# Kernel optimization log

Measured on AMD Instinct MI355X. Metric: run time of the kernel, lower is better.

Reference implementation:

```python
import jax, jax.numpy as jnp
import numpy as np
from jax.scipy.special import erf, erfinv

N_OBS = 8192   # number of observations
N_LOC = 2048   # number of spatial locations (q)


def setup_inputs() -> dict:
    key = jax.random.key(0)
    k1, k2, k3, k4 = jax.random.split(key, 4)
    # random 2-D coordinates -> symmetric pairwise squared-distance matrix (zero diag)
    coords = jax.random.uniform(k1, (N_LOC, 2), dtype=jnp.float32) * 10.0
    dist_matrix = jnp.sum((coords[:, None, :] - coords[None, :, :]) ** 2, axis=-1)  # [q,q]
    Z_idx = jax.random.randint(k2, (N_OBS,), 0, N_LOC)                              # location id per obs
    y_true = jax.random.normal(k3, (N_OBS, 1), dtype=jnp.float32)
    y_pred = jax.random.normal(k4, (N_OBS, 1), dtype=jnp.float32) * 0.5
    return {
        "y_true": y_true,
        "y_pred": y_pred,
        "Z_idx": Z_idx,
        "dist_matrix": dist_matrix,
        "sig2e": jnp.array([1.0], dtype=jnp.float32),
        "sig2bs": jnp.array([0.5], dtype=jnp.float32),
        "lengthscale": jnp.array([2.0], dtype=jnp.float32),
    }


def _inverse_gaussian_cdf(u):
    # tf.math.erfinv(2*clip(u,1e-5,1-1e-5)-1) * sqrt(2)
    return erfinv(2.0 * jnp.clip(u, 1e-5, 1.0 - 1e-5) - 1.0) * jnp.sqrt(2.0)


def reference(y_true, y_pred, Z_idx, dist_matrix, sig2e, sig2bs, lengthscale):
    N = y_true.shape[0]
    q = dist_matrix.shape[0]
    dt = y_true.dtype
    # getD: exponential distance kernel over locations  D = sig2b * exp(-M / (2*ell))
    D = sig2bs[0] * jnp.exp(-dist_matrix / (2.0 * lengthscale[0]))          # [q,q]
    # getZ: dense one-hot design matrix (sparse.to_dense of SparseTensor of ones)
    Z = jax.nn.one_hot(Z_idx, q, dtype=dt)                                   # [N,q]
    # V_batch: V = Z D Z' + sig2e * I
    V = Z @ (D @ Z.T) + sig2e[0] * jnp.eye(N, dtype=dt)                      # [N,N]
    sd = jnp.sqrt(jnp.diagonal(V))                                           # sd_sqrt_V
    R = V / (sd[:, None] * sd[None, :])                                      # correlation matrix
    # Gaussian marginal: sig2 = sig2e + sig2b (diag of V)
    sig2 = sig2e[0] + sig2bs[0]
    resid = y_true - y_pred                                                  # [N,1]
    # distribution.cdf_batch: standard normal CDF of resid / sqrt(sig2)
    u = 0.5 * (erf(resid / jnp.sqrt(2.0 * sig2)) + 1.0)
    m = _inverse_gaussian_cdf(u)                                             # [N,1]
    # distribution.sum_log_pdf_batch: sum of Gaussian log-pdf
    sum_log_pdf = jnp.sum(-0.5 * jnp.log(2.0 * jnp.pi * sig2) - resid ** 2 / (2.0 * sig2))
    # solve + logdet via a single Cholesky of the correlation matrix
    L = jnp.linalg.cholesky(R)
    V_inv_m = jax.scipy.linalg.cho_solve((L, True), m)                       # R^{-1} m
    logdet = 2.0 * jnp.sum(jnp.log(jnp.diagonal(L)))                         # logdet(V) - 2*sum(log sd)
    mV_invm = m.T @ V_inv_m                                                  # [1,1]
    mtm = m.T @ m                                                            # [1,1]
    total_loss = 0.5 * logdet + 0.5 * mV_invm - 0.5 * mtm + 0.5 * sum_log_pdf
    return total_loss  # [1,1]
```

## Files before the change

### kernel.cpp

```cpp
#include <hip/hip_runtime.h>
#include <math.h>

#define Q 2048
#define NOBS 8192

__device__ __forceinline__ float rl(float v, int l) {
  return __int_as_float(__builtin_amdgcn_readlane(__float_as_int(v), l));
}

__device__ __forceinline__ float block_sum256(float v, volatile float* red) {
  int tid = threadIdx.x;
#pragma unroll
  for (int o = 32; o > 0; o >>= 1) v += __shfl_down(v, o);
  __syncthreads();
  if ((tid & 63) == 0) red[tid >> 6] = v;
  __syncthreads();
  return red[0] + red[1] + red[2] + red[3];
}

__device__ __forceinline__ float chol64_reg(float rr[64], int lane) {
  float dv = 1.0f;
#pragma unroll
  for (int j = 0; j < 64; ++j) {
    float vjj = rl(rr[j], j);
    float invd = rsqrtf(vjj);
    float lij = rr[j] * invd;
    rr[j] = lij;
    if (lane == j) dv = lij;
#pragma unroll
    for (int k = j + 1; k < 64; ++k) rr[k] -= lij * rl(lij, k);
  }
  return dv;
}

__global__ __launch_bounds__(256) void obs_kernel(
    const float* __restrict__ yt, const float* __restrict__ yp,
    const int* __restrict__ zidx, const float* __restrict__ s2e_p,
    const float* __restrict__ s2b_p, float* __restrict__ t,
    int* __restrict__ cnt, float* __restrict__ scal) {
  __shared__ float red[4];
  int i = blockIdx.x * 256 + threadIdx.x;
  float s2e = s2e_p[0], s2b = s2b_p[0];
  float sig2 = s2e + s2b;
  float r = yt[i] - yp[i];
  float e = erff(r * rsqrtf(2.0f * sig2));
  float u = 0.5f * (e + 1.0f);
  u = fminf(fmaxf(u, 1e-5f), 1.0f - 1e-5f);
  float m = erfinvf(2.0f * u - 1.0f) * 1.4142135623730951f;
  float slp = -0.5f * logf(2.0f * 3.14159265358979f * sig2) - r * r / (2.0f * sig2);
  int z = zidx[i];
  atomicAdd(&t[z], m);
  atomicAdd(&cnt[z], 1);
  float s1 = block_sum256(slp, red);
  float s2 = block_sum256(m * m, red);
  if (threadIdx.x == 0) {
    atomicAdd(&scal[0], s1);
    atomicAdd(&scal[1], s2);
  }
}

__global__ __launch_bounds__(256) void build_mv(
    const float* __restrict__ dist, const float* __restrict__ s2e_p,
    const float* __restrict__ s2b_p, const float* __restrict__ ell_p,
    const int* __restrict__ cnt, const float* __restrict__ t,
    float* __restrict__ G, float* __restrict__ z, float* __restrict__ scal) {
  __shared__ float red[4];
  int j = blockIdx.x;
  float s2e = s2e_p[0], s2b = s2b_p[0], ell = ell_p[0];
  float sig2 = s2e + s2b;
  float ratio = s2b / sig2;
  float diag = s2e / sig2;
  float inv2ell = 1.0f / (2.0f * ell);
  float cj = (float)cnt[j];
  const float* drow = dist + (size_t)j * Q;
  float* grow = G + (size_t)j * Q;
  float s = 0.0f;
  for (int k = threadIdx.x; k < Q; k += 256) {
    float e = expf(-drow[k] * inv2ell);
    s += e * t[k];
    float g = sqrtf(cj * (float)cnt[k]) * (ratio * e);
    if (j == k) g += diag;
    grow[k] = g;
  }
  float tot = block_sum256(s, red);
  if (threadIdx.x == 0) {
    float wj = ratio * tot;
    z[j] = sqrtf(cj) * wj;
    atomicAdd(&scal[2], t[j] * wj);
  }
}

__global__ __launch_bounds__(256, 1) void estep(
    float* __restrict__ G, float* __restrict__ z, float* __restrict__ scal,
    int j1, int m, int ntile) {
  __shared__ __align__(16) float shA[64 * 68];
  __shared__ __align__(16) float shB[64 * 68];
  __shared__ __align__(16) float LT[64 * 64];
  __shared__ float invDs[64];
  __shared__ float z1s[64];
  __shared__ float z2s[64];
  int tid = threadIdx.x, bx = blockIdx.x;
  int lane = tid & 63;
  int j0 = j1 - 64;
  int tx = tid & 15, ty = tid >> 4;

  if (bx <= m) {
    bool isdiag = (bx == 0);
    int R0 = j1 + bx * 64;

    if (j1 > 0) {
#pragma unroll
      for (int it = 0; it < 4; ++it) {
        int idx = it * 256 + tid;
        int r = idx >> 4, c4 = (idx & 15) * 4;
        float4 v = *(const float4*)(G + (size_t)(j1 + r) * Q + j0 + c4);
        shA[(c4 + 0) * 68 + r] = v.x; shA[(c4 + 1) * 68 + r] = v.y;
        shA[(c4 + 2) * 68 + r] = v.z; shA[(c4 + 3) * 68 + r] = v.w;
        if (!isdiag) {
          float4 u = *(const float4*)(G + (size_t)(R0 + r) * Q + j0 + c4);
          shB[(c4 + 0) * 68 + r] = u.x; shB[(c4 + 1) * 68 + r] = u.y;
          shB[(c4 + 2) * 68 + r] = u.z; shB[(c4 + 3) * 68 + r] = u.w;
        }
      }
      if (isdiag && tid < 64) z1s[tid] = z[j0 + tid];
      __syncthreads();

      float acc1[4][4] = {{0.f}};
      float acc2[4][4] = {{0.f}};
#pragma unroll 8
      for (int p = 0; p < 64; ++p) {
        float4 a4 = *(const float4*)&shA[p * 68 + ty * 4];
        float4 b4 = *(const float4*)&shA[p * 68 + tx * 4];
        float av[4] = {a4.x, a4.y, a4.z, a4.w};
        float bv[4] = {b4.x, b4.y, b4.z, b4.w};
#pragma unroll
        for (int i = 0; i < 4; ++i)
#pragma unroll
          for (int jj = 0; jj < 4; ++jj) acc2[i][jj] += av[i] * bv[jj];
        if (!isdiag) {
          float4 c4v = *(const float4*)&shB[p * 68 + ty * 4];
          float cv[4] = {c4v.x, c4v.y, c4v.z, c4v.w};
#pragma unroll
          for (int i = 0; i < 4; ++i)
#pragma unroll
            for (int jj = 0; jj < 4; ++jj) acc1[i][jj] += cv[i] * bv[jj];
        }
      }
      if (isdiag) {
        int rw = tid >> 2, part = tid & 3;
        float ssum = 0.f;
        for (int p = part; p < 64; p += 4) ssum += shA[p * 68 + rw] * z1s[p];
        ssum += __shfl_down(ssum, 2);
        ssum += __shfl_down(ssum, 1);
        if (part == 0) z2s[rw] = z[j1 + rw] - ssum;
      }
      __syncthreads();

#pragma unroll
      for (int i = 0; i < 4; ++i) {
        float4 g = *(const float4*)(G + (size_t)(j1 + ty * 4 + i) * Q + j1 + tx * 4);
        shA[(ty * 4 + i) * 68 + tx * 4 + 0] = g.x - acc2[i][0];
        shA[(ty * 4 + i) * 68 + tx * 4 + 1] = g.y - acc2[i][1];
        shA[(ty * 4 + i) * 68 + tx * 4 + 2] = g.z - acc2[i][2];
        shA[(ty * 4 + i) * 68 + tx * 4 + 3] = g.w - acc2[i][3];
        if (!isdiag) {
          float4 h = *(const float4*)(G + (size_t)(R0 + ty * 4 + i) * Q + j1 + tx * 4);
          shB[(ty * 4 + i) * 68 + tx * 4 + 0] = h.x - acc1[i][0];
          shB[(ty * 4 + i) * 68 + tx * 4 + 1] = h.y - acc1[i][1];
          shB[(ty * 4 + i) * 68 + tx * 4 + 2] = h.z - acc1[i][2];
          shB[(ty * 4 + i) * 68 + tx * 4 + 3] = h.w - acc1[i][3];
        }
      }
      __syncthreads();
    } else {
#pragma unroll
      for (int it = 0; it < 4; ++it) {
        int idx = it * 256 + tid;
        int r = idx >> 4, c4 = (idx & 15) * 4;
        float4 g = *(const float4*)(G + (size_t)r * Q + c4);
        shA[r * 68 + c4 + 0] = g.x; shA[r * 68 + c4 + 1] = g.y;
        shA[r * 68 + c4 + 2] = g.z; shA[r * 68 + c4 + 3] = g.w;
        if (!isdiag) {
          float4 h = *(const float4*)(G + (size_t)(R0 + r) * Q + c4);
          shB[r * 68 + c4 + 0] = h.x; shB[r * 68 + c4 + 1] = h.y;
          shB[r * 68 + c4 + 2] = h.z; shB[r * 68 + c4 + 3] = h.w;
        }
      }
      if (isdiag && tid < 64) z2s[tid] = z[tid];
      __syncthreads();
    }

    if (tid < 64) {
      float rr[64];
#pragma unroll
      for (int k4 = 0; k4 < 16; ++k4) {
        float4 v = *(const float4*)&shA[lane * 68 + k4 * 4];
        rr[k4 * 4 + 0] = v.x; rr[k4 * 4 + 1] = v.y;
        rr[k4 * 4 + 2] = v.z; rr[k4 * 4 + 3] = v.w;
      }
      __builtin_amdgcn_s_setprio(1);
      float dv = chol64_reg(rr, lane);
      __builtin_amdgcn_s_setprio(0);
      float myinv = 1.0f / dv;
      if (isdiag) {
        float lg = logf(dv);
#pragma unroll
        for (int o = 32; o > 0; o >>= 1) lg += __shfl_down(lg, o);
        if (lane == 0) atomicAdd(&scal[3], lg);
        float a = z2s[lane];
#pragma unroll
        for (int p = 0; p < 64; ++p) {
          float xp = rl(a, p) * rl(myinv, p);
          if (lane > p) a -= xp * rr[p];
        }
        z[j1 + lane] = a * myinv;
      } else {
        invDs[lane] = myinv;
#pragma unroll
        for (int p = 0; p < 64; ++p)
          LT[p * 64 + lane] = (p < lane) ? rr[p] : 0.0f;
        float rr2[64];
#pragma unroll
        for (int k4 = 0; k4 < 16; ++k4) {
          float4 v = *(const float4*)&shB[lane * 68 + k4 * 4];
          rr2[k4 * 4 + 0] = v.x; rr2[k4 * 4 + 1] = v.y;
          rr2[k4 * 4 + 2] = v.z; rr2[k4 * 4 + 3] = v.w;
        }
        __builtin_amdgcn_s_setprio(1);
#pragma unroll
        for (int p = 0; p < 64; ++p) {
          float xp = rr2[p] * invDs[p];
          rr2[p] = xp;
#pragma unroll
          for (int k4 = 0; k4 < 16; ++k4) {
            if (k4 * 4 + 3 > p) {
              float4 l4 = *(const float4*)&LT[p * 64 + k4 * 4];
              rr2[k4 * 4 + 0] -= xp * l4.x;
              rr2[k4 * 4 + 1] -= xp * l4.y;
              rr2[k4 * 4 + 2] -= xp * l4.z;
              rr2[k4 * 4 + 3] -= xp * l4.w;
            }
          }
        }
        __builtin_amdgcn_s_setprio(0);
#pragma unroll
        for (int k4 = 0; k4 < 16; ++k4) {
          float4 st;
          st.x = rr2[k4 * 4 + 0]; st.y = rr2[k4 * 4 + 1];
          st.z = rr2[k4 * 4 + 2]; st.w = rr2[k4 * 4 + 3];
          *(float4*)(G + (size_t)(R0 + lane) * Q + j1 + k4 * 4) = st;
        }
      }
    }
    return;
  }

  int tjob = bx - (m + 1);
  if (tjob < ntile) {
    int bi = (int)((sqrtf(8.0f * (float)tjob + 1.0f) - 1.0f) * 0.5f);
    while ((bi + 1) * (bi + 2) / 2 <= tjob) ++bi;
    while (bi * (bi + 1) / 2 > tjob) --bi;
    int bk = tjob - bi * (bi + 1) / 2;
    int R0 = j1 + 64 + bi * 64, C0 = j1 + 64 + bk * 64;
    bool sym = (bi == bk);
#pragma unroll
    for (int it = 0; it < 4; ++it) {
      int idx = it * 256 + tid;
      int r = idx >> 4, c4 = (idx & 15) * 4;
      float4 v = *(const float4*)(G + (size_t)(R0 + r) * Q + j0 + c4);
      shA[(c4 + 0) * 68 + r] = v.x; shA[(c4 + 1) * 68 + r] = v.y;
      shA[(c4 + 2) * 68 + r] = v.z; shA[(c4 + 3) * 68 + r] = v.w;
      if (!sym) {
        float4 u = *(const float4*)(G + (size_t)(C0 + r) * Q + j0 + c4);
        shB[(c4 + 0) * 68 + r] = u.x; shB[(c4 + 1) * 68 + r] = u.y;
        shB[(c4 + 2) * 68 + r] = u.z; shB[(c4 + 3) * 68 + r] = u.w;
      }
    }
    __syncthreads();
    const float* sB = sym ? shA : shB;
    float acc[4][4] = {{0.f}};
#pragma unroll 8
    for (int p = 0; p < 64; ++p) {
      float4 a4 = *(const float4*)&shA[p * 68 + ty * 4];
      float4 b4 = *(const float4*)&sB[p * 68 + tx * 4];
      float av[4] = {a4.x, a4.y, a4.z, a4.w};
      float bv[4] = {b4.x, b4.y, b4.z, b4.w};
#pragma unroll
      for (int i = 0; i < 4; ++i)
#pragma unroll
        for (int jj = 0; jj < 4; ++jj) acc[i][jj] += av[i] * bv[jj];
    }
#pragma unroll
    for (int i = 0; i < 4; ++i) {
      float* gp = G + (size_t)(R0 + ty * 4 + i) * Q + C0 + tx * 4;
      float4 g = *(const float4*)gp;
      g.x -= acc[i][0]; g.y -= acc[i][1];
      g.z -= acc[i][2]; g.w -= acc[i][3];
      *(float4*)gp = g;
    }
    return;
  }

  {
    int zb = tjob - ntile;
    int B0 = j1 + 64 + zb * 64;
    if (tid < 64) z1s[tid] = z[j0 + tid];
    __syncthreads();
    int rw = tid >> 2, part = tid & 3;
    const float* Lr = G + (size_t)(B0 + rw) * Q + j0;
    float ssum = 0.f;
    for (int p = part; p < 64; p += 4) ssum += Lr[p] * z1s[p];
    ssum += __shfl_down(ssum, 2);
    ssum += __shfl_down(ssum, 1);
    if (part == 0) z[B0 + rw] -= ssum;
  }
}

__global__ __launch_bounds__(256) void final_assemble(
    const float* __restrict__ z, const float* __restrict__ scal,
    const float* __restrict__ s2e_p, const float* __restrict__ s2b_p,
    float* __restrict__ out) {
  __shared__ float red[4];
  int tid = threadIdx.x;
  float bv = 0.f;
  for (int i = tid; i < Q; i += 256) {
    float zi = z[i];
    bv += zi * zi;
  }
  float bvs = block_sum256(bv, red);
  if (tid == 0) {
    float s2e = s2e_p[0], s2b = s2b_p[0];
    float sig2 = s2e + s2b;
    float c = s2e / sig2;
    float slp = scal[0], mtm = scal[1];
    float tw = scal[2], sl = scal[3];
    float tty = (tw - bvs) / c;
    float mrm = (mtm - tty) / c;
    float logdetR = (float)(NOBS - Q) * logf(c) + 2.0f * sl;
    out[0] = 0.5f * logdetR + 0.5f * mrm - 0.5f * mtm + 0.5f * slp;
  }
}

extern "C" void kernel_launch(void* const* d_in, const int* in_sizes, int n_in,
                              void* d_out, int out_size, void* d_ws, size_t ws_size,
                              hipStream_t stream) {
  const float* yt   = (const float*)d_in[0];
  const float* yp   = (const float*)d_in[1];
  const int*   zidx = (const int*)d_in[2];
  const float* dist = (const float*)d_in[3];
  const float* s2e  = (const float*)d_in[4];
  const float* s2b  = (const float*)d_in[5];
  const float* ell  = (const float*)d_in[6];

  float* ws   = (float*)d_ws;
  float* G    = ws;
  float* z    = ws + (size_t)Q * Q;
  float* t    = z + Q;
  int*   cntv = (int*)(t + Q);
  float* scal = t + 2 * Q;

  hipMemsetAsync(t, 0, (2 * Q + 8) * sizeof(float), stream);

  obs_kernel<<<NOBS / 256, 256, 0, stream>>>(yt, yp, zidx, s2e, s2b, t, cntv, scal);
  build_mv<<<Q, 256, 0, stream>>>(dist, s2e, s2b, ell, cntv, t, G, z, scal);

  estep<<<32, 256, 0, stream>>>(G, z, scal, 0, 31, 0);

  for (int s = 0; s <= 30; ++s) {
    int j1 = (s + 1) * 64;
    int m = 30 - s;
    int ntile = m * (m + 1) / 2;
    estep<<<1 + 2 * m + ntile, 256, 0, stream>>>(G, z, scal, j1, m, ntile);
  }

  final_assemble<<<1, 256, 0, stream>>>(z, scal, s2e, s2b, (float*)d_out);
}
```

Baseline: 1.099 ms.

## Restructure blocked Cholesky into right-looking steps with redundant panel solves

```diff
diff --git a/kernel.cpp b/kernel.cpp
--- a/kernel.cpp
+++ b/kernel.cpp
@@ -31,6 +31,47 @@
     for (int k = j + 1; k < 64; ++k) rr[k] -= lij * rl(lij, k);
   }
   return dv;
+}
+
+__device__ __forceinline__ void panel_solve(float* sh, const float* LT,
+                                            const float* invDs, int lane) {
+  float rr2[64];
+#pragma unroll
+  for (int k = 0; k < 64; ++k) rr2[k] = sh[k * 68 + lane];
+  __builtin_amdgcn_s_setprio(1);
+#pragma unroll
+  for (int p = 0; p < 64; ++p) {
+    float xp = rr2[p] * invDs[p];
+    rr2[p] = xp;
+#pragma unroll
+    for (int k4 = 0; k4 < 16; ++k4) {
+      if (k4 * 4 + 3 > p) {
+        float4 l4 = *(const float4*)&LT[p * 64 + k4 * 4];
+        rr2[k4 * 4 + 0] -= xp * l4.x;
+        rr2[k4 * 4 + 1] -= xp * l4.y;
+        rr2[k4 * 4 + 2] -= xp * l4.z;
+        rr2[k4 * 4 + 3] -= xp * l4.w;
+      }
+    }
+  }
+  __builtin_amdgcn_s_setprio(0);
+#pragma unroll
+  for (int k = 0; k < 64; ++k) sh[k * 68 + lane] = rr2[k];
+}
+
+__device__ __forceinline__ void zsolve(const float* LT, const float* invDs,
+                                       const float* zin, float* z1s, int lane) {
+  float rr3[64];
+#pragma unroll
+  for (int p = 0; p < 64; ++p) rr3[p] = LT[p * 64 + lane];
+  float a = zin[lane];
+  float myinv = invDs[lane];
+#pragma unroll
+  for (int p = 0; p < 64; ++p) {
+    float xp = rl(a, p) * rl(myinv, p);
+    if (lane > p) a -= xp * rr3[p];
+  }
+  z1s[lane] = a * myinv;
 }
 
 __global__ __launch_bounds__(256) void obs_kernel(
@@ -90,241 +131,203 @@
   }
 }
 
+__global__ __launch_bounds__(64, 1) void potrf_first(
+    const float* __restrict__ G, float* __restrict__ dsA,
+    float* __restrict__ scal) {
+  int lane = threadIdx.x;
+  float rr[64];
+  const float* row = G + (size_t)lane * Q;
+#pragma unroll
+  for (int k4 = 0; k4 < 16; ++k4) {
+    float4 v = *(const float4*)(row + k4 * 4);
+    rr[k4 * 4 + 0] = v.x; rr[k4 * 4 + 1] = v.y;
+    rr[k4 * 4 + 2] = v.z; rr[k4 * 4 + 3] = v.w;
+  }
+  float dv = chol64_reg(rr, lane);
+#pragma unroll
+  for (int k4 = 0; k4 < 16; ++k4) {
+    float4 st;
+    st.x = rr[k4 * 4 + 0]; st.y = rr[k4 * 4 + 1];
+    st.z = rr[k4 * 4 + 2]; st.w = rr[k4 * 4 + 3];
+    *(float4*)(dsA + lane * 64 + k4 * 4) = st;
+  }
+  float lg = logf(dv);
+#pragma unroll
+  for (int o = 32; o > 0; o >>= 1) lg += __shfl_down(lg, o);
+  if (lane == 0) atomicAdd(&scal[3], lg);
+}
+
 __global__ __launch_bounds__(256, 1) void estep(
-    float* __restrict__ G, float* __restrict__ z, float* __restrict__ scal,
-    int j1, int m, int ntile) {
+    float* __restrict__ G, float* __restrict__ z, float* __restrict__ z1,
+    float* __restrict__ scal, const float* __restrict__ dsR,
+    float* __restrict__ dsW, int j0) {
   __shared__ __align__(16) float shA[64 * 68];
   __shared__ __align__(16) float shB[64 * 68];
   __shared__ __align__(16) float LT[64 * 64];
   __shared__ float invDs[64];
   __shared__ float z1s[64];
-  __shared__ float z2s[64];
   int tid = threadIdx.x, bx = blockIdx.x;
-  int lane = tid & 63;
-  int j0 = j1 - 64;
+  int lane = tid & 63, wv = tid >> 6;
   int tx = tid & 15, ty = tid >> 4;
-
-  if (bx <= m) {
-    bool isdiag = (bx == 0);
-    int R0 = j1 + bx * 64;
-
-    if (j1 > 0) {
-#pragma unroll
-      for (int it = 0; it < 4; ++it) {
-        int idx = it * 256 + tid;
-        int r = idx >> 4, c4 = (idx & 15) * 4;
-        float4 v = *(const float4*)(G + (size_t)(j1 + r) * Q + j0 + c4);
-        shA[(c4 + 0) * 68 + r] = v.x; shA[(c4 + 1) * 68 + r] = v.y;
-        shA[(c4 + 2) * 68 + r] = v.z; shA[(c4 + 3) * 68 + r] = v.w;
-        if (!isdiag) {
-          float4 u = *(const float4*)(G + (size_t)(R0 + r) * Q + j0 + c4);
-          shB[(c4 + 0) * 68 + r] = u.x; shB[(c4 + 1) * 68 + r] = u.y;
-          shB[(c4 + 2) * 68 + r] = u.z; shB[(c4 + 3) * 68 + r] = u.w;
-        }
-      }
-      if (isdiag && tid < 64) z1s[tid] = z[j0 + tid];
-      __syncthreads();
-
-      float acc1[4][4] = {{0.f}};
-      float acc2[4][4] = {{0.f}};
+  int j1 = j0 + 64;
+
+  bool isjob0 = (bx == 0);
+  int tjob = bx - 1;
+  if (!isjob0 && tjob == 0) return;
+
+  int R0, C0;
+  bool sym;
+  if (isjob0) {
+    R0 = j1; C0 = j1; sym = true;
+  } else {
+    int bi = (int)((sqrtf(8.0f * (float)tjob + 1.0f) - 1.0f) * 0.5f);
+    while ((bi + 1) * (bi + 2) / 2 <= tjob) ++bi;
+    while (bi * (bi + 1) / 2 > tjob) --bi;
+    int bk = tjob - bi * (bi + 1) / 2;
+    R0 = j1 + bi * 64; C0 = j1 + bk * 64; sym = (bi == bk);
+  }
+
+#pragma unroll
+  for (int it = 0; it < 4; ++it) {
+    int idx = it * 256 + tid;
+    int r = idx >> 4, c4 = (idx & 15) * 4;
+    float4 v = *(const float4*)(dsR + r * 64 + c4);
+    LT[(c4 + 0) * 64 + r] = (c4 + 0 < r) ? v.x : 0.0f;
+    LT[(c4 + 1) * 64 + r] = (c4 + 1 < r) ? v.y : 0.0f;
+    LT[(c4 + 2) * 64 + r] = (c4 + 2 < r) ? v.z : 0.0f;
+    LT[(c4 + 3) * 64 + r] = (c4 + 3 < r) ? v.w : 0.0f;
+    if (r >= c4 && r < c4 + 4) {
+      float d = (r == c4) ? v.x : (r == c4 + 1) ? v.y : (r == c4 + 2) ? v.z : v.w;
+      invDs[r] = 1.0f / d;
+    }
+  }
+#pragma unroll
+  for (int it = 0; it < 4; ++it) {
+    int idx = it * 256 + tid;
+    int r = idx >> 4, c4 = (idx & 15) * 4;
+    float4 v = *(const float4*)(G + (size_t)(R0 + r) * Q + j0 + c4);
+    shA[(c4 + 0) * 68 + r] = v.x; shA[(c4 + 1) * 68 + r] = v.y;
+    shA[(c4 + 2) * 68 + r] = v.z; shA[(c4 + 3) * 68 + r] = v.w;
+    if (!sym) {
+      float4 u = *(const float4*)(G + (size_t)(C0 + r) * Q + j0 + c4);
+      shB[(c4 + 0) * 68 + r] = u.x; shB[(c4 + 1) * 68 + r] = u.y;
+      shB[(c4 + 2) * 68 + r] = u.z; shB[(c4 + 3) * 68 + r] = u.w;
+    }
+  }
+  __syncthreads();
+
+  if (wv == 0) {
+    panel_solve(shA, LT, invDs, lane);
+  } else if (wv == 1) {
+    if (!sym) panel_solve(shB, LT, invDs, lane);
+    else      zsolve(LT, invDs, z + j0, z1s, lane);
+  }
+  __syncthreads();
+
+  if (isjob0 && wv == 1) z1[j0 + lane] = z1s[lane];
+
+  const float* sB = sym ? shA : shB;
+  float acc[4][4] = {{0.f}};
 #pragma unroll 8
-      for (int p = 0; p < 64; ++p) {
-        float4 a4 = *(const float4*)&shA[p * 68 + ty * 4];
-        float4 b4 = *(const float4*)&shA[p * 68 + tx * 4];
-        float av[4] = {a4.x, a4.y, a4.z, a4.w};
-        float bv[4] = {b4.x, b4.y, b4.z, b4.w};
-#pragma unroll
-        for (int i = 0; i < 4; ++i)
-#pragma unroll
-          for (int jj = 0; jj < 4; ++jj) acc2[i][jj] += av[i] * bv[jj];
-        if (!isdiag) {
-          float4 c4v = *(const float4*)&shB[p * 68 + ty * 4];
-          float cv[4] = {c4v.x, c4v.y, c4v.z, c4v.w};
-#pragma unroll
-          for (int i = 0; i < 4; ++i)
-#pragma unroll
-            for (int jj = 0; jj < 4; ++jj) acc1[i][jj] += cv[i] * bv[jj];
-        }
-      }
-      if (isdiag) {
-        int rw = tid >> 2, part = tid & 3;
-        float ssum = 0.f;
-        for (int p = part; p < 64; p += 4) ssum += shA[p * 68 + rw] * z1s[p];
-        ssum += __shfl_down(ssum, 2);
-        ssum += __shfl_down(ssum, 1);
-        if (part == 0) z2s[rw] = z[j1 + rw] - ssum;
-      }
-      __syncthreads();
-
-#pragma unroll
-      for (int i = 0; i < 4; ++i) {
-        float4 g = *(const float4*)(G + (size_t)(j1 + ty * 4 + i) * Q + j1 + tx * 4);
-        shA[(ty * 4 + i) * 68 + tx * 4 + 0] = g.x - acc2[i][0];
-        shA[(ty * 4 + i) * 68 + tx * 4 + 1] = g.y - acc2[i][1];
-        shA[(ty * 4 + i) * 68 + tx * 4 + 2] = g.z - acc2[i][2];
-        shA[(ty * 4 + i) * 68 + tx * 4 + 3] = g.w - acc2[i][3];
-        if (!isdiag) {
-          float4 h = *(const float4*)(G + (size_t)(R0 + ty * 4 + i) * Q + j1 + tx * 4);
-          shB[(ty * 4 + i) * 68 + tx * 4 + 0] = h.x - acc1[i][0];
-          shB[(ty * 4 + i) * 68 + tx * 4 + 1] = h.y - acc1[i][1];
-          shB[(ty * 4 + i) * 68 + tx * 4 + 2] = h.z - acc1[i][2];
-          shB[(ty * 4 + i) * 68 + tx * 4 + 3] = h.w - acc1[i][3];
-        }
-      }
-      __syncthreads();
-    } else {
-#pragma unroll
-      for (int it = 0; it < 4; ++it) {
-        int idx = it * 256 + tid;
-        int r = idx >> 4, c4 = (idx & 15) * 4;
-        float4 g = *(const float4*)(G + (size_t)r * Q + c4);
-        shA[r * 68 + c4 + 0] = g.x; shA[r * 68 + c4 + 1] = g.y;
-        shA[r * 68 + c4 + 2] = g.z; shA[r * 68 + c4 + 3] = g.w;
-        if (!isdiag) {
-          float4 h = *(const float4*)(G + (size_t)(R0 + r) * Q + c4);
-          shB[r * 68 + c4 + 0] = h.x; shB[r * 68 + c4 + 1] = h.y;
-          shB[r * 68 + c4 + 2] = h.z; shB[r * 68 + c4 + 3] = h.w;
-        }
-      }
-      if (isdiag && tid < 64) z2s[tid] = z[tid];
-      __syncthreads();
-    }
-
-    if (tid < 64) {
+  for (int p = 0; p < 64; ++p) {
+    float4 a4 = *(const float4*)&shA[p * 68 + ty * 4];
+    float4 b4 = *(const float4*)&sB[p * 68 + tx * 4];
+    float av[4] = {a4.x, a4.y, a4.z, a4.w};
+    float bv[4] = {b4.x, b4.y, b4.z, b4.w};
+#pragma unroll
+    for (int i = 0; i < 4; ++i)
+#pragma unroll
+      for (int jj = 0; jj < 4; ++jj) acc[i][jj] += av[i] * bv[jj];
+  }
+
+  if (isjob0) {
+#pragma unroll
+    for (int i = 0; i < 4; ++i) {
+      const float* gp = G + (size_t)(j1 + ty * 4 + i) * Q + j1 + tx * 4;
+      float4 g = *(const float4*)gp;
+      shB[(ty * 4 + i) * 68 + tx * 4 + 0] = g.x - acc[i][0];
+      shB[(ty * 4 + i) * 68 + tx * 4 + 1] = g.y - acc[i][1];
+      shB[(ty * 4 + i) * 68 + tx * 4 + 2] = g.z - acc[i][2];
+      shB[(ty * 4 + i) * 68 + tx * 4 + 3] = g.w - acc[i][3];
+    }
+    __syncthreads();
+    if (wv == 0) {
       float rr[64];
 #pragma unroll
       for (int k4 = 0; k4 < 16; ++k4) {
-        float4 v = *(const float4*)&shA[lane * 68 + k4 * 4];
+        float4 v = *(const float4*)&shB[lane * 68 + k4 * 4];
         rr[k4 * 4 + 0] = v.x; rr[k4 * 4 + 1] = v.y;
         rr[k4 * 4 + 2] = v.z; rr[k4 * 4 + 3] = v.w;
       }
       __builtin_amdgcn_s_setprio(1);
       float dv = chol64_reg(rr, lane);
       __builtin_amdgcn_s_setprio(0);
-      float myinv = 1.0f / dv;
-      if (isdiag) {
-        float lg = logf(dv);
-#pragma unroll
-        for (int o = 32; o > 0; o >>= 1) lg += __shfl_down(lg, o);
-        if (lane == 0) atomicAdd(&scal[3], lg);
-        float a = z2s[lane];
-#pragma unroll
-        for (int p = 0; p < 64; ++p) {
-          float xp = rl(a, p) * rl(myinv, p);
-          if (lane > p) a -= xp * rr[p];
-        }
-        z[j1 + lane] = a * myinv;
-      } else {
-        invDs[lane] = myinv;
-#pragma unroll
-        for (int p = 0; p < 64; ++p)
-          LT[p * 64 + lane] = (p < lane) ? rr[p] : 0.0f;
-        float rr2[64];
-#pragma unroll
-        for (int k4 = 0; k4 < 16; ++k4) {
-          float4 v = *(const float4*)&shB[lane * 68 + k4 * 4];
-          rr2[k4 * 4 + 0] = v.x; rr2[k4 * 4 + 1] = v.y;
-          rr2[k4 * 4 + 2] = v.z; rr2[k4 * 4 + 3] = v.w;
-        }
-        __builtin_amdgcn_s_setprio(1);
-#pragma unroll
-        for (int p = 0; p < 64; ++p) {
-          float xp = rr2[p] * invDs[p];
-          rr2[p] = xp;
-#pragma unroll
-          for (int k4 = 0; k4 < 16; ++k4) {
-            if (k4 * 4 + 3 > p) {
-              float4 l4 = *(const float4*)&LT[p * 64 + k4 * 4];
-              rr2[k4 * 4 + 0] -= xp * l4.x;
-              rr2[k4 * 4 + 1] -= xp * l4.y;
-              rr2[k4 * 4 + 2] -= xp * l4.z;
-              rr2[k4 * 4 + 3] -= xp * l4.w;
-            }
-          }
-        }
-        __builtin_amdgcn_s_setprio(0);
-#pragma unroll
-        for (int k4 = 0; k4 < 16; ++k4) {
-          float4 st;
-          st.x = rr2[k4 * 4 + 0]; st.y = rr2[k4 * 4 + 1];
-          st.z = rr2[k4 * 4 + 2]; st.w = rr2[k4 * 4 + 3];
-          *(float4*)(G + (size_t)(R0 + lane) * Q + j1 + k4 * 4) = st;
-        }
+#pragma unroll
+      for (int k4 = 0; k4 < 16; ++k4) {
+        float4 st;
+        st.x = rr[k4 * 4 + 0]; st.y = rr[k4 * 4 + 1];
+        st.z = rr[k4 * 4 + 2]; st.w = rr[k4 * 4 + 3];
+        *(float4*)(dsW + lane * 64 + k4 * 4) = st;
       }
+      float lg = logf(dv);
+#pragma unroll
+      for (int o = 32; o > 0; o >>= 1) lg += __shfl_down(lg, o);
+      if (lane == 0) atomicAdd(&scal[3], lg);
+    } else if (wv == 1) {
+      float zs = 0.f;
+#pragma unroll 8
+      for (int p = 0; p < 64; ++p) zs += shA[p * 68 + lane] * z1s[p];
+      z[j1 + lane] -= zs;
     }
     return;
   }
 
-  int tjob = bx - (m + 1);
-  if (tjob < ntile) {
-    int bi = (int)((sqrtf(8.0f * (float)tjob + 1.0f) - 1.0f) * 0.5f);
-    while ((bi + 1) * (bi + 2) / 2 <= tjob) ++bi;
-    while (bi * (bi + 1) / 2 > tjob) --bi;
-    int bk = tjob - bi * (bi + 1) / 2;
-    int R0 = j1 + 64 + bi * 64, C0 = j1 + 64 + bk * 64;
-    bool sym = (bi == bk);
-#pragma unroll
-    for (int it = 0; it < 4; ++it) {
-      int idx = it * 256 + tid;
-      int r = idx >> 4, c4 = (idx & 15) * 4;
-      float4 v = *(const float4*)(G + (size_t)(R0 + r) * Q + j0 + c4);
-      shA[(c4 + 0) * 68 + r] = v.x; shA[(c4 + 1) * 68 + r] = v.y;
-      shA[(c4 + 2) * 68 + r] = v.z; shA[(c4 + 3) * 68 + r] = v.w;
-      if (!sym) {
-        float4 u = *(const float4*)(G + (size_t)(C0 + r) * Q + j0 + c4);
-        shB[(c4 + 0) * 68 + r] = u.x; shB[(c4 + 1) * 68 + r] = u.y;
-        shB[(c4 + 2) * 68 + r] = u.z; shB[(c4 + 3) * 68 + r] = u.w;
-      }
-    }
-    __syncthreads();
-    const float* sB = sym ? shA : shB;
-    float acc[4][4] = {{0.f}};
+  if (sym && wv == 0) {
+    float zs = 0.f;
 #pragma unroll 8
-    for (int p = 0; p < 64; ++p) {
-      float4 a4 = *(const float4*)&shA[p * 68 + ty * 4];
-      float4 b4 = *(const float4*)&sB[p * 68 + tx * 4];
-      float av[4] = {a4.x, a4.y, a4.z, a4.w};
-      float bv[4] = {b4.x, b4.y, b4.z, b4.w};
-#pragma unroll
-      for (int i = 0; i < 4; ++i)
-#pragma unroll
-        for (int jj = 0; jj < 4; ++jj) acc[i][jj] += av[i] * bv[jj];
-    }
-#pragma unroll
-    for (int i = 0; i < 4; ++i) {
-      float* gp = G + (size_t)(R0 + ty * 4 + i) * Q + C0 + tx * 4;
-      float4 g = *(const float4*)gp;
-      g.x -= acc[i][0]; g.y -= acc[i][1];
-      g.z -= acc[i][2]; g.w -= acc[i][3];
-      *(float4*)gp = g;
-    }
-    return;
-  }
-
-  {
-    int zb = tjob - ntile;
-    int B0 = j1 + 64 + zb * 64;
-    if (tid < 64) z1s[tid] = z[j0 + tid];
-    __syncthreads();
-    int rw = tid >> 2, part = tid & 3;
-    const float* Lr = G + (size_t)(B0 + rw) * Q + j0;
-    float ssum = 0.f;
-    for (int p = part; p < 64; p += 4) ssum += Lr[p] * z1s[p];
-    ssum += __shfl_down(ssum, 2);
-    ssum += __shfl_down(ssum, 1);
-    if (part == 0) z[B0 + rw] -= ssum;
+    for (int p = 0; p < 64; ++p) zs += shA[p * 68 + lane] * z1s[p];
+    z[R0 + lane] -= zs;
+  }
+#pragma unroll
+  for (int i = 0; i < 4; ++i) {
+    float* gp = G + (size_t)(R0 + ty * 4 + i) * Q + C0 + tx * 4;
+    float4 g = *(const float4*)gp;
+    g.x -= acc[i][0]; g.y -= acc[i][1];
+    g.z -= acc[i][2]; g.w -= acc[i][3];
+    *(float4*)gp = g;
   }
 }
 
 __global__ __launch_bounds__(256) void final_assemble(
-    const float* __restrict__ z, const float* __restrict__ scal,
+    const float* __restrict__ z, const float* __restrict__ z1,
+    const float* __restrict__ ds31, const float* __restrict__ scal,
     const float* __restrict__ s2e_p, const float* __restrict__ s2b_p,
     float* __restrict__ out) {
   __shared__ float red[4];
+  __shared__ float z1last[64];
   int tid = threadIdx.x;
+  if (tid < 64) {
+    int lane = tid;
+    float rr3[64];
+#pragma unroll
+    for (int k4 = 0; k4 < 16; ++k4) {
+      float4 v = *(const float4*)(ds31 + lane * 64 + k4 * 4);
+      rr3[k4 * 4 + 0] = v.x; rr3[k4 * 4 + 1] = v.y;
+      rr3[k4 * 4 + 2] = v.z; rr3[k4 * 4 + 3] = v.w;
+    }
+    float myinv = 1.0f / rr3[lane];
+    float a = z[Q - 64 + lane];
+#pragma unroll
+    for (int p = 0; p < 64; ++p) {
+      float xp = rl(a, p) * rl(myinv, p);
+      if (lane > p) a -= xp * rr3[p];
+    }
+    z1last[lane] = a * myinv;
+  }
+  __syncthreads();
   float bv = 0.f;
   for (int i = tid; i < Q; i += 256) {
-    float zi = z[i];
+    float zi = (i < Q - 64) ? z1[i] : z1last[i - (Q - 64)];
     bv += zi * zi;
   }
   float bvs = block_sum256(bv, red);
@@ -358,20 +361,25 @@
   float* t    = z + Q;
   int*   cntv = (int*)(t + Q);
   float* scal = t + 2 * Q;
+  float* z1   = scal + 8;
+  float* dsA  = z1 + Q;
+  float* dsB  = dsA + 4096;
 
   hipMemsetAsync(t, 0, (2 * Q + 8) * sizeof(float), stream);
 
   obs_kernel<<<NOBS / 256, 256, 0, stream>>>(yt, yp, zidx, s2e, s2b, t, cntv, scal);
   build_mv<<<Q, 256, 0, stream>>>(dist, s2e, s2b, ell, cntv, t, G, z, scal);
 
-  estep<<<32, 256, 0, stream>>>(G, z, scal, 0, 31, 0);
+  potrf_first<<<1, 64, 0, stream>>>(G, dsA, scal);
 
   for (int s = 0; s <= 30; ++s) {
-    int j1 = (s + 1) * 64;
-    int m = 30 - s;
+    int m = 31 - s;
     int ntile = m * (m + 1) / 2;
-    estep<<<1 + 2 * m + ntile, 256, 0, stream>>>(G, z, scal, j1, m, ntile);
-  }
-
-  final_assemble<<<1, 256, 0, stream>>>(z, scal, s2e, s2b, (float*)d_out);
-}
+    const float* dsR = (s & 1) ? dsB : dsA;
+    float* dsW = (s & 1) ? dsA : dsB;
+    estep<<<1 + ntile, 256, 0, stream>>>(G, z, z1, scal, dsR, dsW, s * 64);
+  }
+
+  final_assemble<<<1, 256, 0, stream>>>(z, z1, dsB, scal, s2e, s2b,
+                                        (float*)d_out);
+}
```

Result: faster. 973.6 us (-11.4%).
